# Optimization experiments

Measured on AMD Instinct MI355X. Metric: run time of the kernel, lower is better.

The kernel has to match this reference:

```python
import jax, jax.numpy as jnp
import numpy as np

RADIUS = 2
SIGMA_SPATIAL = 2.5
SIGMA_RANGE_FACTOR = 0.5


def setup_inputs() -> dict:
    key = jax.random.key(0)
    k1, k2 = jax.random.split(key)
    source = jax.random.normal(k1, (4, 64, 64, 64), dtype=jnp.float32)
    guidance = jax.random.uniform(k2, (4, 3, 256, 256), dtype=jnp.float32)
    return {"source": source, "guidance": guidance}


def _jbu(source, guidance):
    # source: [B, C, h, w] low-res features; guidance: [B, Cg, H, W] high-res image
    B, C, h, w = source.shape
    _, Cg, H, W = guidance.shape
    s = H // h  # integer upsampling factor
    r = RADIUS

    # per-batch range sigma from guidance std (torch.std is unbiased -> ddof=1)
    sigma_range = SIGMA_RANGE_FACTOR * jnp.std(guidance, axis=(1, 2, 3), ddof=1)  # [B]
    inv_2sr2 = 1.0 / (2.0 * sigma_range * sigma_range)  # [B]
    inv_2ss2 = 1.0 / (2.0 * SIGMA_SPATIAL * SIGMA_SPATIAL)

    # guidance sampled at low-res cell centers: [B, Cg, h, w]
    off = s // 2
    g_low = guidance[:, :, off::s, off::s]

    # low-res center index for every hi-res pixel
    yc = jnp.arange(H) // s  # [H]
    xc = jnp.arange(W) // s  # [W]

    num = jnp.zeros((B, C, H, W), dtype=source.dtype)
    den = jnp.zeros((B, 1, H, W), dtype=source.dtype)

    # fixed small (2r+1)^2 = 25 window taps; unrolled loop, each tap is a
    # clamped gather + fused weight compute + accumulate (no huge intermediates)
    for dy in range(-r, r + 1):
        yi = jnp.clip(yc + dy, 0, h - 1)  # [H]
        for dx in range(-r, r + 1):
            xi = jnp.clip(xc + dx, 0, w - 1)  # [W]
            src_g = source[:, :, yi[:, None], xi[None, :]]  # [B, C, H, W]
            g_g = g_low[:, :, yi[:, None], xi[None, :]]      # [B, Cg, H, W]
            diff2 = jnp.sum((guidance - g_g) ** 2, axis=1)   # [B, H, W]
            w_range = jnp.exp(-diff2 * inv_2sr2[:, None, None])
            w_spatial = np.exp(-(dy * dy + dx * dx) * 1.0) ** 0.0  # placeholder removed below
            w_spatial = jnp.exp(jnp.asarray(-(dy * dy + dx * dx) * inv_2ss2, dtype=source.dtype))
            wgt = (w_spatial * w_range)[:, None]  # [B, 1, H, W]
            num = num + src_g * wgt
            den = den + wgt

    return num / (den + 1e-8)


def reference(source, guidance):
    return _jbu(source, guidance)
```

## Files before the change

kernel.cpp:

```cpp
#include <hip/hip_runtime.h>

#define B_  4
#define C_  64
#define H_  256
#define W_  256
#define h_  64
#define w_  64
#define L2SW2 (-0.46166241f)
#define L2SW1 (-0.11541560f)

__global__ void jbu_stats(const float* __restrict__ g, double* __restrict__ stats) {
    int b     = blockIdx.x >> 5;
    int slice = blockIdx.x & 31;
    const float4* p = (const float4*)(g + (size_t)b * 3 * H_ * W_) + (size_t)slice * 1536;
    double s = 0.0, s2 = 0.0;
    for (int i = threadIdx.x; i < 1536; i += 256) {
        float4 v = p[i];
        s  += (double)v.x + (double)v.y + (double)v.z + (double)v.w;
        s2 += (double)v.x * v.x + (double)v.y * v.y
            + (double)v.z * v.z + (double)v.w * v.w;
    }
    for (int off = 32; off > 0; off >>= 1) {
        s  += __shfl_down(s,  off);
        s2 += __shfl_down(s2, off);
    }
    __shared__ double ls[8];
    int wid  = threadIdx.x >> 6;
    int lane = threadIdx.x & 63;
    if (lane == 0) { ls[wid] = s; ls[4 + wid] = s2; }
    __syncthreads();
    if (threadIdx.x == 0) {
        stats[blockIdx.x]       = ls[0] + ls[1] + ls[2] + ls[3];
        stats[128 + blockIdx.x] = ls[4] + ls[5] + ls[6] + ls[7];
    }
}

__global__ __launch_bounds__(256, 4)
void jbu_mega16(const float* __restrict__ src, const float* __restrict__ guid,
                const double* __restrict__ stats, float* __restrict__ out) {
    __shared__ __align__(16) float sS[5 * 64 * 20];
    __shared__ __align__(16) float sG[5 * 64 * 4];

    int cg  = blockIdx.x & 3;
    int y4  = (blockIdx.x >> 2) & 63;
    int b   = blockIdx.x >> 8;
    int tid = threadIdx.x;

    double S = 0.0, S2 = 0.0;
    for (int i = 0; i < 32; ++i) {
        S  += stats[b * 32 + i];
        S2 += stats[128 + b * 32 + i];
    }
    const double n = 3.0 * H_ * W_;
    double var = (S2 - S * S / n) / (n - 1.0);
    float invrl2 = (float)(2.0 / var) * 1.44269504f;

    int yi[5];
    #pragma unroll
    for (int d = 0; d < 5; ++d) {
        int u = y4 + d - 2;
        yi[d] = u < 0 ? 0 : (u > h_ - 1 ? h_ - 1 : u);
    }

    const float* sb = src + ((size_t)b * C_ + cg * 16) * h_ * w_;
    {
        int xx0 = tid & 63;
        int j4  = ((tid >> 6) & 3) * 4;
        #pragma unroll
        for (int it = 0; it < 5; ++it) {
            int yy = yi[it];
            float4 v;
            v.x = sb[((size_t)(j4 + 0) * h_ + yy) * w_ + xx0];
            v.y = sb[((size_t)(j4 + 1) * h_ + yy) * w_ + xx0];
            v.z = sb[((size_t)(j4 + 2) * h_ + yy) * w_ + xx0];
            v.w = sb[((size_t)(j4 + 3) * h_ + yy) * w_ + xx0];
            *(float4*)&sS[(it * 64 + xx0) * 20 + j4] = v;
        }
    }
    for (int k = tid; k < 320; k += 256) {
        int xx  = k & 63;
        int row = k >> 6;
        int u   = y4 + row - 2;
        int yy  = u < 0 ? 0 : (u > h_ - 1 ? h_ - 1 : u);
        const float* gbase = guid + (size_t)b * 3 * H_ * W_
                           + (size_t)(yy * 4 + 2) * W_ + (xx * 4 + 2);
        float gx = gbase[0];
        float gy = gbase[H_ * W_];
        float gz = gbase[2 * H_ * W_];
        float ss = fmaf(gz, gz, fmaf(gy, gy, gx * gx));
        float4 e = make_float4(gx, gy, gz, -invrl2 * ss);
        *(float4*)&sG[(row * 64 + xx) * 4] = e;
    }

    __syncthreads();

    int x  = tid;
    int y0 = y4 * 4;

    float gp[4][3];
    float A[4];
    #pragma unroll
    for (int c = 0; c < 3; ++c)
        #pragma unroll
        for (int p = 0; p < 4; ++p)
            gp[p][c] = guid[(((size_t)b * 3 + c) * H_ + (y0 + p)) * W_ + x];
    float t2 = 2.0f * invrl2;
    #pragma unroll
    for (int p = 0; p < 4; ++p) {
        float ss = fmaf(gp[p][2], gp[p][2], fmaf(gp[p][1], gp[p][1], gp[p][0] * gp[p][0]));
        A[p] = -invrl2 * ss;
        gp[p][0] *= t2; gp[p][1] *= t2; gp[p][2] *= t2;
    }

    int xb = x >> 2;
    int xi[5];
    #pragma unroll
    for (int d = 0; d < 5; ++d) {
        int v = xb + d - 2;
        xi[d] = v < 0 ? 0 : (v > w_ - 1 ? w_ - 1 : v);
    }

    const float l2sw[5] = {L2SW2, L2SW1, 0.0f, L2SW1, L2SW2};

    float acc[4][16];
    float den[4];
    #pragma unroll
    for (int p = 0; p < 4; ++p) {
        den[p] = 0.0f;
        #pragma unroll
        for (int c = 0; c < 16; ++c) acc[p][c] = 0.0f;
    }

    #pragma unroll
    for (int dy = 0; dy < 5; ++dy) {
        float l2y = l2sw[dy];
        int   rb  = dy * 64;
        #pragma unroll
        for (int dx = 0; dx < 5; ++dx) {
            int xx = xi[dx];
            float4 gl = *(const float4*)&sG[(rb + xx) * 4];
            float ct = gl.w + (l2y + l2sw[dx]);
            float wgt[4];
            #pragma unroll
            for (int p = 0; p < 4; ++p) {
                float m = fmaf(gp[p][2], gl.z,
                          fmaf(gp[p][1], gl.y, gp[p][0] * gl.x));
                float wv = __builtin_amdgcn_exp2f(m + ct + A[p]);
                wgt[p] = wv;
                den[p] += wv;
            }
            const float* sP = &sS[(rb + xx) * 20];
            #pragma unroll
            for (int q = 0; q < 4; ++q) {
                float4 sv = *(const float4*)(sP + q * 4);
                #pragma unroll
                for (int p = 0; p < 4; ++p) {
                    acc[p][q * 4 + 0] = fmaf(wgt[p], sv.x, acc[p][q * 4 + 0]);
                    acc[p][q * 4 + 1] = fmaf(wgt[p], sv.y, acc[p][q * 4 + 1]);
                    acc[p][q * 4 + 2] = fmaf(wgt[p], sv.z, acc[p][q * 4 + 2]);
                    acc[p][q * 4 + 3] = fmaf(wgt[p], sv.w, acc[p][q * 4 + 3]);
                }
            }
        }
    }

    float* ob = out + ((size_t)b * C_ + cg * 16) * H_ * W_;
    #pragma unroll
    for (int p = 0; p < 4; ++p) {
        float r = 1.0f / (den[p] + 1e-8f);
        int row = (y0 + p) * W_ + x;
        #pragma unroll
        for (int c = 0; c < 16; ++c) {
            ob[(size_t)c * H_ * W_ + row] = acc[p][c] * r;
        }
    }
}

extern "C" void kernel_launch(void* const* d_in, const int* in_sizes, int n_in,
                              void* d_out, int out_size, void* d_ws, size_t ws_size,
                              hipStream_t stream) {
    const float* src  = (const float*)d_in[0];
    const float* guid = (const float*)d_in[1];
    float* out = (float*)d_out;

    double* stats = (double*)d_ws;

    jbu_stats<<<128, 256, 0, stream>>>(guid, stats);
    jbu_mega16<<<B_ * 64 * 4, 256, 0, stream>>>(src, guid, stats, out);
}
```

Measured before the change: 95.88 us.

## Use packed FMA accumulation, nontemporal stores, fewer stats blocks, deferred sigma

The inner accumulation now uses inline v_pk_fma_f32 on two-wide vectors, so each instruction does two FMAs. The range-weight exponent folds into a single FMA chain, and the sigma-dependent scaling of the cached guidance term moves into the loop. The stats kernel drops from 128 to 32 blocks, and each main-kernel block reduces only 8 partials, read after the shared-memory loads are issued. Output stores become nontemporal. Fewer stats blocks mean less parallelism for the reduction, and the inline asm limits the compiler's scheduling.

```diff
diff --git a/kernel.cpp b/kernel.cpp
--- a/kernel.cpp
+++ b/kernel.cpp
@@ -9,12 +9,14 @@
 #define L2SW2 (-0.46166241f)
 #define L2SW1 (-0.11541560f)
 
+typedef float v2f __attribute__((ext_vector_type(2)));
+
 __global__ void jbu_stats(const float* __restrict__ g, double* __restrict__ stats) {
-    int b     = blockIdx.x >> 5;
-    int slice = blockIdx.x & 31;
-    const float4* p = (const float4*)(g + (size_t)b * 3 * H_ * W_) + (size_t)slice * 1536;
+    int b     = blockIdx.x >> 3;
+    int slice = blockIdx.x & 7;
+    const float4* p = (const float4*)(g + (size_t)b * 3 * H_ * W_) + (size_t)slice * 6144;
     double s = 0.0, s2 = 0.0;
-    for (int i = threadIdx.x; i < 1536; i += 256) {
+    for (int i = threadIdx.x; i < 6144; i += 256) {
         float4 v = p[i];
         s  += (double)v.x + (double)v.y + (double)v.z + (double)v.w;
         s2 += (double)v.x * v.x + (double)v.y * v.y
@@ -30,8 +32,8 @@
     if (lane == 0) { ls[wid] = s; ls[4 + wid] = s2; }
     __syncthreads();
     if (threadIdx.x == 0) {
-        stats[blockIdx.x]       = ls[0] + ls[1] + ls[2] + ls[3];
-        stats[128 + blockIdx.x] = ls[4] + ls[5] + ls[6] + ls[7];
+        stats[blockIdx.x]      = ls[0] + ls[1] + ls[2] + ls[3];
+        stats[32 + blockIdx.x] = ls[4] + ls[5] + ls[6] + ls[7];
     }
 }
 
@@ -45,15 +47,6 @@
     int y4  = (blockIdx.x >> 2) & 63;
     int b   = blockIdx.x >> 8;
     int tid = threadIdx.x;
-
-    double S = 0.0, S2 = 0.0;
-    for (int i = 0; i < 32; ++i) {
-        S  += stats[b * 32 + i];
-        S2 += stats[128 + b * 32 + i];
-    }
-    const double n = 3.0 * H_ * W_;
-    double var = (S2 - S * S / n) / (n - 1.0);
-    float invrl2 = (float)(2.0 / var) * 1.44269504f;
 
     int yi[5];
     #pragma unroll
@@ -88,15 +81,22 @@
         float gy = gbase[H_ * W_];
         float gz = gbase[2 * H_ * W_];
         float ss = fmaf(gz, gz, fmaf(gy, gy, gx * gx));
-        float4 e = make_float4(gx, gy, gz, -invrl2 * ss);
+        float4 e = make_float4(gx, gy, gz, ss);
         *(float4*)&sG[(row * 64 + xx) * 4] = e;
     }
 
-    __syncthreads();
+    double S = 0.0, S2 = 0.0;
+    for (int i = 0; i < 8; ++i) {
+        S  += stats[b * 8 + i];
+        S2 += stats[32 + b * 8 + i];
+    }
+    const double n = 3.0 * H_ * W_;
+    double var = (S2 - S * S / n) / (n - 1.0);
+    float invrl2 = (float)(2.0 / var) * 1.44269504f;
+    float ninv   = -invrl2;
 
     int x  = tid;
     int y0 = y4 * 4;
-
     float gp[4][3];
     float A[4];
     #pragma unroll
@@ -112,6 +112,8 @@
         gp[p][0] *= t2; gp[p][1] *= t2; gp[p][2] *= t2;
     }
 
+    __syncthreads();
+
     int xb = x >> 2;
     int xi[5];
     #pragma unroll
@@ -122,13 +124,13 @@
 
     const float l2sw[5] = {L2SW2, L2SW1, 0.0f, L2SW1, L2SW2};
 
-    float acc[4][16];
+    v2f accv[4][8];
     float den[4];
     #pragma unroll
     for (int p = 0; p < 4; ++p) {
         den[p] = 0.0f;
         #pragma unroll
-        for (int c = 0; c < 16; ++c) acc[p][c] = 0.0f;
+        for (int j = 0; j < 8; ++j) { accv[p][j].x = 0.0f; accv[p][j].y = 0.0f; }
     }
 
     #pragma unroll
@@ -139,26 +141,28 @@
         for (int dx = 0; dx < 5; ++dx) {
             int xx = xi[dx];
             float4 gl = *(const float4*)&sG[(rb + xx) * 4];
-            float ct = gl.w + (l2y + l2sw[dx]);
-            float wgt[4];
+            float ct = fmaf(gl.w, ninv, l2y + l2sw[dx]);
+            v2f w2[4];
             #pragma unroll
             for (int p = 0; p < 4; ++p) {
                 float m = fmaf(gp[p][2], gl.z,
-                          fmaf(gp[p][1], gl.y, gp[p][0] * gl.x));
-                float wv = __builtin_amdgcn_exp2f(m + ct + A[p]);
-                wgt[p] = wv;
+                          fmaf(gp[p][1], gl.y,
+                          fmaf(gp[p][0], gl.x, ct + A[p])));
+                float wv = __builtin_amdgcn_exp2f(m);
+                w2[p].x = wv; w2[p].y = wv;
                 den[p] += wv;
             }
             const float* sP = &sS[(rb + xx) * 20];
             #pragma unroll
             for (int q = 0; q < 4; ++q) {
-                float4 sv = *(const float4*)(sP + q * 4);
+                v2f lo = *(const v2f*)(sP + q * 4);
+                v2f hi = *(const v2f*)(sP + q * 4 + 2);
                 #pragma unroll
                 for (int p = 0; p < 4; ++p) {
-                    acc[p][q * 4 + 0] = fmaf(wgt[p], sv.x, acc[p][q * 4 + 0]);
-                    acc[p][q * 4 + 1] = fmaf(wgt[p], sv.y, acc[p][q * 4 + 1]);
-                    acc[p][q * 4 + 2] = fmaf(wgt[p], sv.z, acc[p][q * 4 + 2]);
-                    acc[p][q * 4 + 3] = fmaf(wgt[p], sv.w, acc[p][q * 4 + 3]);
+                    asm("v_pk_fma_f32 %0, %1, %2, %0"
+                        : "+v"(accv[p][q * 2 + 0]) : "v"(w2[p]), "v"(lo));
+                    asm("v_pk_fma_f32 %0, %1, %2, %0"
+                        : "+v"(accv[p][q * 2 + 1]) : "v"(w2[p]), "v"(hi));
                 }
             }
         }
@@ -170,8 +174,9 @@
         float r = 1.0f / (den[p] + 1e-8f);
         int row = (y0 + p) * W_ + x;
         #pragma unroll
-        for (int c = 0; c < 16; ++c) {
-            ob[(size_t)c * H_ * W_ + row] = acc[p][c] * r;
+        for (int j = 0; j < 8; ++j) {
+            __builtin_nontemporal_store(accv[p][j].x * r, &ob[(size_t)(2 * j + 0) * H_ * W_ + row]);
+            __builtin_nontemporal_store(accv[p][j].y * r, &ob[(size_t)(2 * j + 1) * H_ * W_ + row]);
         }
     }
 }
@@ -185,6 +190,6 @@
 
     double* stats = (double*)d_ws;
 
-    jbu_stats<<<128, 256, 0, stream>>>(guid, stats);
+    jbu_stats<<<32, 256, 0, stream>>>(guid, stats);
     jbu_mega16<<<B_ * 64 * 4, 256, 0, stream>>>(src, guid, stats, out);
 }
```

Measured after the change: 98.13 us. 1.02x slower.
